# Optimization experiments

Hardware: AMD Instinct MI355X
Metric: run time of the kernel (lower is better)

## Reference

```python
import jax, jax.numpy as jnp
import numpy as np

DIM = 1024
INNER = DIM // 2
DSTATE = 8
KSZ = 3
DTRANK = max(INNER // 8, 4)
B, L = 4, 4096


def setup_inputs() -> dict:
    key = jax.random.key(0)
    ks = jax.random.split(key, 8)
    s = 0.02
    x = jax.random.normal(ks[0], (B, L, DIM), dtype=jnp.float32)
    W_in = jax.random.normal(ks[1], (DIM, DIM), dtype=jnp.float32) * s
    Kx = jax.random.normal(ks[2], (INNER, 1, KSZ), dtype=jnp.float32) * 0.1
    Kz = jax.random.normal(ks[3], (INNER, 1, KSZ), dtype=jnp.float32) * 0.1
    W_xproj = jax.random.normal(ks[4], (DTRANK + 2 * DSTATE, INNER), dtype=jnp.float32) * s
    W_dt = jax.random.normal(ks[5], (INNER, DTRANK), dtype=jnp.float32) * s
    # dt bias: inverse_softplus of exp(linspace(log dt_min, log dt_max))
    dt_init = jnp.exp(jnp.linspace(jnp.log(0.02), jnp.log(0.2), INNER))
    b_dt = jnp.log(jnp.expm1(dt_init)).astype(jnp.float32)
    A_log = jnp.log(jnp.tile(jnp.arange(1, DSTATE + 1, dtype=jnp.float32), (INNER, 1)))
    D = jnp.ones((INNER,), dtype=jnp.float32)
    W_out = jax.random.normal(ks[6], (DIM, DIM), dtype=jnp.float32) * s
    return {"x": x, "W_in": W_in, "Kx": Kx, "Kz": Kz, "W_xproj": W_xproj,
            "W_dt": W_dt, "b_dt": b_dt, "A_log": A_log, "D": D, "W_out": W_out}


def _dwconv_silu(u, kern):
    # u: [B,L,C], kern: [C,1,K] depthwise (groups=C), 'same' padding
    c = u.shape[-1]
    v = jnp.transpose(u, (0, 2, 1))  # [B,C,L]
    v = jax.lax.conv_general_dilated(v, kern, (1,), [(KSZ // 2, KSZ // 2)],
                                     dimension_numbers=("NCH", "OIH", "NCH"),
                                     feature_group_count=c)
    return jax.nn.silu(jnp.transpose(v, (0, 2, 1)))


def _forward(x, W_in, Kx, Kz, W_xproj, W_dt, b_dt, A_log, D, W_out):
    h = jnp.einsum("bld,ed->ble", x, W_in)  # Linear(dim,dim), no bias
    xb, zb = jnp.split(h, 2, axis=-1)       # [B,L,INNER] each
    xb = _dwconv_silu(xb, Kx)
    zb = _dwconv_silu(zb, Kz)
    proj = jnp.einsum("blc,oc->blo", xb, W_xproj)
    dt_raw = proj[..., :DTRANK]
    b_raw = proj[..., DTRANK:DTRANK + DSTATE]
    c_raw = proj[..., DTRANK + DSTATE:]
    delta = jnp.clip(jax.nn.softplus(jnp.einsum("blr,cr->blc", dt_raw, W_dt) + b_dt), 1e-4, 1.0)  # [B,L,C]
    b_term = jnp.tanh(b_raw)  # [B,L,N]
    c_term = jnp.tanh(c_raw)  # [B,L,N]
    a = jax.nn.softplus(A_log) + 1e-4  # [C,N]
    decay = jnp.clip(jnp.exp(-delta[..., None] * a), 1e-4, 1.0)        # [B,L,C,N]
    drive = (1.0 - decay) * (b_term[:, :, None, :] * xb[..., None])    # [B,L,C,N]

    def step(state, inp):
        dec_t, drv_t, c_t, x_t = inp  # [B,C,N], [B,C,N], [B,N], [B,C]
        state = dec_t * state + drv_t
        y = jnp.sum(state * c_t[:, None, :], axis=-1) + D * x_t  # [B,C]
        return state, y

    tm = lambda t: jnp.moveaxis(t, 1, 0)  # time-major
    state0 = jnp.zeros((x.shape[0], INNER, DSTATE), dtype=jnp.float32)
    _, ys = jax.lax.scan(step, state0, (tm(decay), tm(drive), tm(c_term), tm(xb)))
    y = jnp.moveaxis(ys, 0, 1)  # [B,L,INNER]
    return jnp.einsum("bld,ed->ble", jnp.concatenate([y, zb], axis=-1), W_out)


def reference(x, W_in, Kx, Kz, W_xproj, W_dt, b_dt, A_log, D, W_out):
    return _forward(x, W_in, Kx, Kz, W_xproj, W_dt, b_dt, A_log, D, W_out)
```

## Files before the change

### kernel.cpp

```cpp
#include <hip/hip_runtime.h>


using bf16x8 = __attribute__((ext_vector_type(8))) short;
using f32x4  = __attribute__((ext_vector_type(4))) float;

__device__ __forceinline__ unsigned short f2bf(float f) {
  unsigned int u = __float_as_uint(f);
  u = u + 0x7fffu + ((u >> 16) & 1u);
  return (unsigned short)(u >> 16);
}

__device__ __forceinline__ float fsoftplus(float x) {
  return (x > 15.f) ? x : __logf(1.f + __expf(x));
}

__device__ __forceinline__ float ftanh(float x) {
  float v = fminf(fmaxf(x, -15.f), 15.f);
  float e = __expf(2.f * v);
  return (e - 1.f) / (e + 1.f);
}

__global__ __launch_bounds__(256) void cvt_bf16_kernel(
    const float* __restrict__ in, unsigned short* __restrict__ out, int n4) {
  int i = blockIdx.x * 256 + threadIdx.x;
  if (i < n4) {
    float4 v = ((const float4*)in)[i];
    ushort4 o;
    o.x = f2bf(v.x); o.y = f2bf(v.y); o.z = f2bf(v.z); o.w = f2bf(v.w);
    ((ushort4*)out)[i] = o;
  }
}

__global__ __launch_bounds__(256) void cvt_wxp_kernel(
    const float* __restrict__ Wx, unsigned short* __restrict__ out) {
  int i = blockIdx.x * 256 + threadIdx.x;
  int row = i >> 9;
  out[i] = (row < 80) ? f2bf(Wx[i]) : (unsigned short)0;
}

__global__ __launch_bounds__(256) void gemm_bt_bf16(
    const unsigned short* __restrict__ A,
    const unsigned short* __restrict__ B,
    float* __restrict__ C, int M, int N, int K) {
  __shared__ short As[128 * 32];
  __shared__ short Bs[128 * 32];
  const int m0 = blockIdx.x * 128;
  const int n0 = blockIdx.y * 128;
  const int lane = threadIdx.x & 63;
  const int wv = threadIdx.x >> 6;
  const int wm = (wv >> 1) * 64;
  const int wn = (wv & 1) * 64;
  f32x4 acc[4][4] = {};
  const int row_a = wv * 32 + (lane >> 2);
  const int koff = (lane & 3) * 8;
  const unsigned short* gA = A + (size_t)(m0 + row_a) * K + koff;
  const unsigned short* gB = B + (size_t)(n0 + row_a) * K + koff;
  short* lA = &As[(wv * 32) * 32];
  short* lB = &Bs[(wv * 32) * 32];
  const int r = lane & 15;
  const int q = lane >> 4;
  for (int k0 = 0; k0 < K; k0 += 32) {
    __syncthreads();
    __builtin_amdgcn_global_load_lds((const __attribute__((address_space(1))) void*)(const void*)gA,
                                     (__attribute__((address_space(3))) void*)(void*)lA, 16, 0, 0);
    __builtin_amdgcn_global_load_lds((const __attribute__((address_space(1))) void*)(const void*)(gA + 16 * K),
                                     (__attribute__((address_space(3))) void*)(void*)(lA + 16 * 32), 16, 0, 0);
    __builtin_amdgcn_global_load_lds((const __attribute__((address_space(1))) void*)(const void*)gB,
                                     (__attribute__((address_space(3))) void*)(void*)lB, 16, 0, 0);
    __builtin_amdgcn_global_load_lds((const __attribute__((address_space(1))) void*)(const void*)(gB + 16 * K),
                                     (__attribute__((address_space(3))) void*)(void*)(lB + 16 * 32), 16, 0, 0);
    gA += 32; gB += 32;
    __syncthreads();
    bf16x8 av[4], bv[4];
#pragma unroll
    for (int i = 0; i < 4; ++i)
      av[i] = *(const bf16x8*)&As[(wm + i * 16 + r) * 32 + q * 8];
#pragma unroll
    for (int j = 0; j < 4; ++j)
      bv[j] = *(const bf16x8*)&Bs[(wn + j * 16 + r) * 32 + q * 8];
#pragma unroll
    for (int i = 0; i < 4; ++i)
#pragma unroll
      for (int j = 0; j < 4; ++j)
        acc[i][j] = __builtin_amdgcn_mfma_f32_16x16x32_bf16(av[i], bv[j], acc[i][j], 0, 0, 0);
  }
#pragma unroll
  for (int i = 0; i < 4; ++i)
#pragma unroll
    for (int j = 0; j < 4; ++j)
#pragma unroll
      for (int t = 0; t < 4; ++t)
        C[(size_t)(m0 + wm + i * 16 + q * 4 + t) * N + (n0 + wn + j * 16 + r)] = acc[i][j][t];
}

__device__ __forceinline__ void g256_stage(short* lds, int slot,
    const unsigned short* sp, int ktIdx, int wvLds) {
  const unsigned short* s = sp + ktIdx * 64;
  __builtin_amdgcn_global_load_lds((const __attribute__((address_space(1))) void*)s,
      (__attribute__((address_space(3))) void*)(lds + slot * 8192 + wvLds), 16, 0, 0);
  __builtin_amdgcn_global_load_lds((const __attribute__((address_space(1))) void*)(s + 32),
      (__attribute__((address_space(3))) void*)(lds + slot * 8192 + 4096 + wvLds), 16, 0, 0);
}

template <int PAR, int MH, int NHLO, bool RA, bool RB, int SSLOT, bool VM, bool HINT>
__device__ __forceinline__ void g256_phase(
    short* lds, int aSlotOff, int bSlotOff, int aoff, int boff, int wvLds,
    bf16x8 (&av)[4][2], bf16x8 (&bv)[4][2], f32x4 (&acc)[8][4],
    const unsigned short* sp, int ktIdx) {
  if (RA) {
#pragma unroll
    for (int ii = 0; ii < 4; ++ii)
#pragma unroll
      for (int ks = 0; ks < 2; ++ks)
        av[ii][ks] = *(const bf16x8*)&lds[PAR * 4 * 8192 + aSlotOff + ks * 4096 +
                                          (MH * 4 + ii) * 512 + aoff];
  }
  if (RB) {
#pragma unroll
    for (int jj = 0; jj < 2; ++jj)
#pragma unroll
      for (int ks = 0; ks < 2; ++ks)
        bv[NHLO + jj][ks] = *(const bf16x8*)&lds[(PAR * 4 + 2) * 8192 + bSlotOff + ks * 4096 +
                                                 (NHLO + jj) * 512 + boff];
  }
  g256_stage(lds, SSLOT, sp, ktIdx, wvLds);
  if (HINT) asm volatile("s_waitcnt lgkmcnt(8)");
  if (VM) asm volatile("s_waitcnt vmcnt(4)" ::: "memory");
  __builtin_amdgcn_s_barrier();
  asm volatile("s_waitcnt lgkmcnt(0)" ::: "memory");
  __builtin_amdgcn_s_setprio(1);
#pragma unroll
  for (int ii = 0; ii < 4; ++ii)
#pragma unroll
    for (int jj = 0; jj < 2; ++jj) {
      acc[MH * 4 + ii][NHLO + jj] = __builtin_amdgcn_mfma_f32_16x16x32_bf16(
          av[ii][0], bv[NHLO + jj][0], acc[MH * 4 + ii][NHLO + jj], 0, 0, 0);
      acc[MH * 4 + ii][NHLO + jj] = __builtin_amdgcn_mfma_f32_16x16x32_bf16(
          av[ii][1], bv[NHLO + jj][1], acc[MH * 4 + ii][NHLO + jj], 0, 0, 0);
    }
  __builtin_amdgcn_s_setprio(0);
  __builtin_amdgcn_s_barrier();
}

__global__ __launch_bounds__(512, 2) void gemm256_bt(
    const unsigned short* __restrict__ A,
    const unsigned short* __restrict__ B,
    float* __restrict__ C, int M, int N, int K) {
  __shared__ short lds[8 * 8192];
  const int nmt = M >> 8;
  const int bid = blockIdx.x;
  const int swz = (bid & 7) * ((int)gridDim.x >> 3) + (bid >> 3);
  const int mtile = swz % nmt, ntile = swz / nmt;
  const int m0 = mtile << 8, n0 = ntile << 8;
  const int tid = threadIdx.x;
  const int w = tid >> 6, lane = tid & 63;
  const int r = lane & 15, q = lane >> 4;
  const int wrow = w >> 2, wcol = w & 3;
  const int trow = tid >> 2, tcol = (tid & 3) << 3;
  const unsigned short* pA0 = A + (size_t)(m0 + trow) * K + tcol;
  const unsigned short* pA1 = pA0 + (size_t)128 * K;
  const unsigned short* pB0 = B + (size_t)(n0 + trow) * K + tcol;
  const unsigned short* pB1 = pB0 + (size_t)128 * K;
  const int wvLds = w * 512;
  const int aSlotOff = wrow * 8192;
  const int bSlotOff = (wcol >> 1) * 8192;
  const int aoff = r * 32 + q * 8;
  const int boff = (wcol & 1) * 2048 + r * 32 + q * 8;
  bf16x8 av[4][2], bv[4][2];
  f32x4 acc[8][4] = {};
  const int NT = K >> 6;
  const int NI = NT >> 1;
  g256_stage(lds, 0, pA0, 0, wvLds);
  g256_stage(lds, 1, pA1, 0, wvLds);
  g256_stage(lds, 2, pB0, 0, wvLds);
  g256_stage(lds, 3, pB1, 0, wvLds);
  g256_stage(lds, 6, pB0, 1, wvLds);
  g256_stage(lds, 7, pB1, 1, wvLds);
  asm volatile("s_waitcnt vmcnt(4)" ::: "memory");
  __builtin_amdgcn_s_barrier();
#pragma unroll 1
  for (int it = 0; it < NI; ++it) {
    const int ktO  = 2 * it + 1;
    const int ktE2 = (2 * it + 2 < NT) ? 2 * it + 2 : NT - 1;
    const int ktO2 = (2 * it + 3 < NT) ? 2 * it + 3 : NT - 1;
    g256_phase<0, 0, 0, true,  true,  4, false, true >(lds, aSlotOff, bSlotOff, aoff, boff, wvLds, av, bv, acc, pA0, ktO);
    g256_phase<0, 0, 2, false, true,  5, false, false>(lds, aSlotOff, bSlotOff, aoff, boff, wvLds, av, bv, acc, pA1, ktO);
    g256_phase<0, 1, 2, true,  false, 2, false, false>(lds, aSlotOff, bSlotOff, aoff, boff, wvLds, av, bv, acc, pB0, ktE2);
    g256_phase<0, 1, 0, false, false, 0, true,  false>(lds, aSlotOff, bSlotOff, aoff, boff, wvLds, av, bv, acc, pA0, ktE2);
    g256_phase<1, 0, 0, true,  true,  1, false, true >(lds, aSlotOff, bSlotOff, aoff, boff, wvLds, av, bv, acc, pA1, ktE2);
    g256_phase<1, 0, 2, false, true,  3, false, false>(lds, aSlotOff, bSlotOff, aoff, boff, wvLds, av, bv, acc, pB1, ktE2);
    g256_phase<1, 1, 2, true,  false, 6, false, false>(lds, aSlotOff, bSlotOff, aoff, boff, wvLds, av, bv, acc, pB0, ktO2);
    g256_phase<1, 1, 0, false, false, 7, true,  false>(lds, aSlotOff, bSlotOff, aoff, boff, wvLds, av, bv, acc, pB1, ktO2);
  }
  asm volatile("s_waitcnt vmcnt(0) lgkmcnt(0)" ::: "memory");
  float* Cw = C + (size_t)(m0 + wrow * 128) * N + n0 + wcol * 64;
#pragma unroll
  for (int ii = 0; ii < 8; ++ii)
#pragma unroll
    for (int jj = 0; jj < 4; ++jj)
#pragma unroll
      for (int t = 0; t < 4; ++t)
        Cw[(size_t)(ii * 16 + q * 4 + t) * N + jj * 16 + r] = acc[ii][jj][t];
}

__global__ __launch_bounds__(256) void conv_silu_kernel(
    const float* __restrict__ h, const float* __restrict__ Kx, const float* __restrict__ Kz,
    float* __restrict__ xb, unsigned short* __restrict__ xbbf,
    unsigned short* __restrict__ cat) {
  int tid = blockIdx.x * 256 + threadIdx.x;
  int ch = tid & 1023;
  int bl = tid >> 10;
  int l = bl & 4095;
  float k0, k1, k2;
  int c;
  if (ch < 512) { c = ch;       k0 = Kx[c * 3]; k1 = Kx[c * 3 + 1]; k2 = Kx[c * 3 + 2]; }
  else          { c = ch - 512; k0 = Kz[c * 3]; k1 = Kz[c * 3 + 1]; k2 = Kz[c * 3 + 2]; }
  size_t idx = (size_t)bl * 1024 + ch;
  float um = (l > 0)    ? h[idx - 1024] : 0.f;
  float u0 = h[idx];
  float up = (l < 4095) ? h[idx + 1024] : 0.f;
  float v = um * k0 + u0 * k1 + up * k2;
  float o = v / (1.f + __expf(-v));
  if (ch < 512) { xb[(size_t)bl * 512 + c] = o; xbbf[(size_t)bl * 512 + c] = f2bf(o); }
  else          cat[idx] = f2bf(o);
}

__global__ __launch_bounds__(256) void prep_dtbc_kernel(
    const float* __restrict__ proj, unsigned short* __restrict__ dtr,
    float* __restrict__ bterm, float* __restrict__ cterm) {
  int i = blockIdx.x * 256 + threadIdx.x;
  int row = i >> 7, col = i & 127;
  float v = proj[i];
  if (col < 64)      dtr[row * 64 + col] = f2bf(v);
  else if (col < 72) bterm[row * 8 + (col - 64)] = ftanh(v);
  else if (col < 80) cterm[row * 8 + (col - 72)] = ftanh(v);
}

__global__ __launch_bounds__(256) void scan_p1(
    const float* __restrict__ draw, const float* __restrict__ bterm,
    const float* __restrict__ xb, const float* __restrict__ A_log,
    const float* __restrict__ bdt,
    float* __restrict__ Aprod, float* __restrict__ Bpart) {
  int tid = threadIdx.x;
  int gid = blockIdx.x;
  int chunk = gid & 127, half = (gid >> 7) & 1, b = gid >> 8;
  int c = half * 256 + tid;
  float4 a0 = *(const float4*)&A_log[c * 8];
  float4 a1 = *(const float4*)&A_log[c * 8 + 4];
  float na[8] = {a0.x, a0.y, a0.z, a0.w, a1.x, a1.y, a1.z, a1.w};
#pragma unroll
  for (int s = 0; s < 8; ++s) na[s] = -(fsoftplus(na[s]) + 1e-4f);
  float bb = bdt[c];
  int l0 = chunk * 32;
  size_t base  = ((size_t)b * 4096 + l0) * 512 + c;
  size_t bbase = ((size_t)b * 4096 + l0) * 8;
  float S[8] = {}, Ap[8] = {1.f, 1.f, 1.f, 1.f, 1.f, 1.f, 1.f, 1.f};
  for (int i = 0; i < 32; ++i) {
    float dr = draw[base] + bb;
    float xv = xb[base];
    float delta = fminf(fmaxf(fsoftplus(dr), 1e-4f), 1.f);
    float4 bt0 = *(const float4*)&bterm[bbase];
    float4 bt1 = *(const float4*)&bterm[bbase + 4];
    float bt[8] = {bt0.x, bt0.y, bt0.z, bt0.w, bt1.x, bt1.y, bt1.z, bt1.w};
#pragma unroll
    for (int s = 0; s < 8; ++s) {
      float dec = fminf(fmaxf(__expf(delta * na[s]), 1e-4f), 1.f);
      float btx = bt[s] * xv;
      S[s] = dec * S[s] + (btx - dec * btx);
      Ap[s] *= dec;
    }
    base += 512; bbase += 8;
  }
  size_t o = (size_t)chunk * 16384 + ((size_t)(b * 512 + c)) * 8;
  *(float4*)&Aprod[o]     = make_float4(Ap[0], Ap[1], Ap[2], Ap[3]);
  *(float4*)&Aprod[o + 4] = make_float4(Ap[4], Ap[5], Ap[6], Ap[7]);
  *(float4*)&Bpart[o]     = make_float4(S[0], S[1], S[2], S[3]);
  *(float4*)&Bpart[o + 4] = make_float4(S[4], S[5], S[6], S[7]);
}

__global__ __launch_bounds__(256) void scan_p2(
    const float* __restrict__ Aprod, const float* __restrict__ Bpart,
    float* __restrict__ initst) {
  int t = blockIdx.x * 256 + threadIdx.x;
  float st = 0.f;
  for (int ch = 0; ch < 128; ++ch) {
    size_t o = (size_t)ch * 16384 + t;
    initst[o] = st;
    st = Aprod[o] * st + Bpart[o];
  }
}

__global__ __launch_bounds__(256) void scan_p3(
    const float* __restrict__ draw, const float* __restrict__ bterm,
    const float* __restrict__ cterm, const float* __restrict__ xb,
    const float* __restrict__ A_log, const float* __restrict__ bdt,
    const float* __restrict__ Dp,
    const float* __restrict__ initst, unsigned short* __restrict__ cat) {
  int tid = threadIdx.x;
  int gid = blockIdx.x;
  int chunk = gid & 127, half = (gid >> 7) & 1, b = gid >> 8;
  int c = half * 256 + tid;
  float4 a0 = *(const float4*)&A_log[c * 8];
  float4 a1 = *(const float4*)&A_log[c * 8 + 4];
  float na[8] = {a0.x, a0.y, a0.z, a0.w, a1.x, a1.y, a1.z, a1.w};
#pragma unroll
  for (int s = 0; s < 8; ++s) na[s] = -(fsoftplus(na[s]) + 1e-4f);
  float bb = bdt[c];
  float Dv = Dp[c];
  size_t o = (size_t)chunk * 16384 + ((size_t)(b * 512 + c)) * 8;
  float4 s0 = *(const float4*)&initst[o];
  float4 s1 = *(const float4*)&initst[o + 4];
  float S[8] = {s0.x, s0.y, s0.z, s0.w, s1.x, s1.y, s1.z, s1.w};
  int l0 = chunk * 32;
  size_t base  = ((size_t)b * 4096 + l0) * 512 + c;
  size_t bbase = ((size_t)b * 4096 + l0) * 8;
  size_t cbase = ((size_t)b * 4096 + l0) * 1024 + c;
  for (int i = 0; i < 32; ++i) {
    float dr = draw[base] + bb;
    float xv = xb[base];
    float delta = fminf(fmaxf(fsoftplus(dr), 1e-4f), 1.f);
    float4 bt0 = *(const float4*)&bterm[bbase];
    float4 bt1 = *(const float4*)&bterm[bbase + 4];
    float4 ct0 = *(const float4*)&cterm[bbase];
    float4 ct1 = *(const float4*)&cterm[bbase + 4];
    float bt[8] = {bt0.x, bt0.y, bt0.z, bt0.w, bt1.x, bt1.y, bt1.z, bt1.w};
    float ct[8] = {ct0.x, ct0.y, ct0.z, ct0.w, ct1.x, ct1.y, ct1.z, ct1.w};
    float acc = Dv * xv;
#pragma unroll
    for (int s = 0; s < 8; ++s) {
      float dec = fminf(fmaxf(__expf(delta * na[s]), 1e-4f), 1.f);
      float btx = bt[s] * xv;
      S[s] = dec * S[s] + (btx - dec * btx);
      acc += S[s] * ct[s];
    }
    cat[cbase] = f2bf(acc);
    base += 512; bbase += 8; cbase += 1024;
  }
}

extern "C" void kernel_launch(void* const* d_in, const int* in_sizes, int n_in,
                              void* d_out, int out_size, void* d_ws, size_t ws_size,
                              hipStream_t stream) {
  (void)in_sizes; (void)n_in; (void)out_size; (void)ws_size;
  const float* x       = (const float*)d_in[0];
  const float* W_in    = (const float*)d_in[1];
  const float* Kx      = (const float*)d_in[2];
  const float* Kz      = (const float*)d_in[3];
  const float* W_xproj = (const float*)d_in[4];
  const float* W_dt    = (const float*)d_in[5];
  const float* b_dt    = (const float*)d_in[6];
  const float* A_log   = (const float*)d_in[7];
  const float* Dp      = (const float*)d_in[8];
  const float* W_out   = (const float*)d_in[9];
  float* out = (float*)d_out;

  char* w = (char*)d_ws;
  unsigned short* xbf  = (unsigned short*)(w);
  float* xb    = (float*)(w + 33554432);
  float* draw  = (float*)(w + 67108864);
  float* bterm = (float*)(w + 100663296);
  float* cterm = (float*)(w + 101187584);
  float* Aprod = (float*)(w + 101711872);
  float* Bpart = (float*)(w + 110100480);
  float* initst = (float*)(w + 118489088);
  unsigned short* winbf  = (unsigned short*)(w + 126877696);
  unsigned short* woutbf = (unsigned short*)(w + 128974848);
  unsigned short* dtr    = (unsigned short*)(w + 131072000);
  unsigned short* wxp_bf = (unsigned short*)(w + 133169152);
  unsigned short* wd_bf  = (unsigned short*)(w + 133300224);
  unsigned short* xbbf = (unsigned short*)Aprod;
  float* proj = draw;
  float* h = out;

  cvt_bf16_kernel<<<16384, 256, 0, stream>>>(x, xbf, 4194304);
  cvt_bf16_kernel<<<1024, 256, 0, stream>>>(W_in, winbf, 262144);
  cvt_bf16_kernel<<<1024, 256, 0, stream>>>(W_out, woutbf, 262144);
  cvt_bf16_kernel<<<32, 256, 0, stream>>>(W_dt, wd_bf, 8192);
  cvt_wxp_kernel<<<256, 256, 0, stream>>>(W_xproj, wxp_bf);

  gemm256_bt<<<256, 512, 0, stream>>>(xbf, winbf, h, 16384, 1024, 1024);

  conv_silu_kernel<<<65536, 256, 0, stream>>>(h, Kx, Kz, xb, xbbf, xbf );

  gemm_bt_bf16<<<dim3(128, 1), 256, 0, stream>>>(xbbf, wxp_bf, proj, 16384, 128, 512);
  prep_dtbc_kernel<<<8192, 256, 0, stream>>>(proj, dtr, bterm, cterm);
  gemm_bt_bf16<<<dim3(128, 4), 256, 0, stream>>>(dtr, wd_bf, draw, 16384, 512, 64);

  scan_p1<<<1024, 256, 0, stream>>>(draw, bterm, xb, A_log, b_dt, Aprod, Bpart);
  scan_p2<<<64, 256, 0, stream>>>(Aprod, Bpart, initst);
  scan_p3<<<1024, 256, 0, stream>>>(draw, bterm, cterm, xb, A_log, b_dt, Dp, initst, xbf );

  gemm256_bt<<<256, 512, 0, stream>>>(xbf, woutbf, out, 16384, 1024, 1024);
}
```

Measured before the change: 351.6 us.

## Swizzle LDS layout for 256-tile GEMM staging and remap tiles per XCD

The GEMM staging now loads full 64-wide K rows per thread group and XOR-swizzles the column chunk by row. The fragment reads apply the matching swizzle, which is meant to cut LDS bank conflicts on the bf16x8 reads and make the global loads more contiguous. Block-to-tile mapping changes so each XCD owns a contiguous band of M tiles, aiming for better L2 reuse. This assumes nmt is divisible by 8, and the new layout has to stay exactly consistent between the stage and read paths.

```diff
diff --git a/kernel.cpp b/kernel.cpp
--- a/kernel.cpp
+++ b/kernel.cpp
@@ -94,11 +94,11 @@
 }
 
 __device__ __forceinline__ void g256_stage(short* lds, int slot,
-    const unsigned short* sp, int ktIdx, int wvLds) {
+    const unsigned short* sp, int ktIdx, int wvLds, int K) {
   const unsigned short* s = sp + ktIdx * 64;
   __builtin_amdgcn_global_load_lds((const __attribute__((address_space(1))) void*)s,
       (__attribute__((address_space(3))) void*)(lds + slot * 8192 + wvLds), 16, 0, 0);
-  __builtin_amdgcn_global_load_lds((const __attribute__((address_space(1))) void*)(s + 32),
+  __builtin_amdgcn_global_load_lds((const __attribute__((address_space(1))) void*)(s + (size_t)64 * K),
       (__attribute__((address_space(3))) void*)(lds + slot * 8192 + 4096 + wvLds), 16, 0, 0);
 }
 
@@ -106,24 +106,22 @@
 __device__ __forceinline__ void g256_phase(
     short* lds, int aSlotOff, int bSlotOff, int aoff, int boff, int wvLds,
     bf16x8 (&av)[4][2], bf16x8 (&bv)[4][2], f32x4 (&acc)[8][4],
-    const unsigned short* sp, int ktIdx) {
+    const unsigned short* sp, int ktIdx, int K) {
   if (RA) {
 #pragma unroll
-    for (int ii = 0; ii < 4; ++ii)
-#pragma unroll
-      for (int ks = 0; ks < 2; ++ks)
-        av[ii][ks] = *(const bf16x8*)&lds[PAR * 4 * 8192 + aSlotOff + ks * 4096 +
-                                          (MH * 4 + ii) * 512 + aoff];
+    for (int ii = 0; ii < 4; ++ii) {
+      av[ii][0] = *(const bf16x8*)&lds[PAR * 4 * 8192 + aSlotOff + MH * 4096 + ii * 1024 + aoff];
+      av[ii][1] = *(const bf16x8*)&lds[PAR * 4 * 8192 + aSlotOff + MH * 4096 + ii * 1024 + (aoff ^ 32)];
+    }
   }
   if (RB) {
 #pragma unroll
-    for (int jj = 0; jj < 2; ++jj)
-#pragma unroll
-      for (int ks = 0; ks < 2; ++ks)
-        bv[NHLO + jj][ks] = *(const bf16x8*)&lds[(PAR * 4 + 2) * 8192 + bSlotOff + ks * 4096 +
-                                                 (NHLO + jj) * 512 + boff];
-  }
-  g256_stage(lds, SSLOT, sp, ktIdx, wvLds);
+    for (int jj = 0; jj < 2; ++jj) {
+      bv[NHLO + jj][0] = *(const bf16x8*)&lds[(PAR * 4 + 2) * 8192 + bSlotOff + (NHLO + jj) * 1024 + boff];
+      bv[NHLO + jj][1] = *(const bf16x8*)&lds[(PAR * 4 + 2) * 8192 + bSlotOff + (NHLO + jj) * 1024 + (boff ^ 32)];
+    }
+  }
+  g256_stage(lds, SSLOT, sp, ktIdx, wvLds, K);
   if (HINT) asm volatile("s_waitcnt lgkmcnt(8)");
   if (VM) asm volatile("s_waitcnt vmcnt(4)" ::: "memory");
   __builtin_amdgcn_s_barrier();
@@ -149,33 +147,38 @@
   __shared__ short lds[8 * 8192];
   const int nmt = M >> 8;
   const int bid = blockIdx.x;
-  const int swz = (bid & 7) * ((int)gridDim.x >> 3) + (bid >> 3);
-  const int mtile = swz % nmt, ntile = swz / nmt;
+  const int g = nmt >> 3;
+  const int xcd = bid & 7;
+  const int loc = bid >> 3;
+  const int mtile = xcd * g + (loc % g);
+  const int ntile = loc / g;
   const int m0 = mtile << 8, n0 = ntile << 8;
   const int tid = threadIdx.x;
   const int w = tid >> 6, lane = tid & 63;
   const int r = lane & 15, q = lane >> 4;
   const int wrow = w >> 2, wcol = w & 3;
-  const int trow = tid >> 2, tcol = (tid & 3) << 3;
-  const unsigned short* pA0 = A + (size_t)(m0 + trow) * K + tcol;
-  const unsigned short* pA1 = pA0 + (size_t)128 * K;
-  const unsigned short* pB0 = B + (size_t)(n0 + trow) * K + tcol;
-  const unsigned short* pB1 = pB0 + (size_t)128 * K;
+  const int srow = tid >> 3;
+  const int scol = ((tid & 7) ^ (srow & 7)) << 3;
+  const unsigned short* pA0 = A + (size_t)(m0 + srow) * K + scol;
+  const unsigned short* pA1 = A + (size_t)(m0 + 128 + srow) * K + scol;
+  const unsigned short* pB0 = B + (size_t)(n0 + srow) * K + scol;
+  const unsigned short* pB1 = B + (size_t)(n0 + 128 + srow) * K + scol;
   const int wvLds = w * 512;
   const int aSlotOff = wrow * 8192;
   const int bSlotOff = (wcol >> 1) * 8192;
-  const int aoff = r * 32 + q * 8;
-  const int boff = (wcol & 1) * 2048 + r * 32 + q * 8;
+  const int swzc = (q * 8) ^ ((r & 7) << 3);
+  const int aoff = r * 64 + swzc;
+  const int boff = (wcol & 1) * 4096 + r * 64 + swzc;
   bf16x8 av[4][2], bv[4][2];
   f32x4 acc[8][4] = {};
   const int NT = K >> 6;
   const int NI = NT >> 1;
-  g256_stage(lds, 0, pA0, 0, wvLds);
-  g256_stage(lds, 1, pA1, 0, wvLds);
-  g256_stage(lds, 2, pB0, 0, wvLds);
-  g256_stage(lds, 3, pB1, 0, wvLds);
-  g256_stage(lds, 6, pB0, 1, wvLds);
-  g256_stage(lds, 7, pB1, 1, wvLds);
+  g256_stage(lds, 0, pA0, 0, wvLds, K);
+  g256_stage(lds, 1, pA1, 0, wvLds, K);
+  g256_stage(lds, 2, pB0, 0, wvLds, K);
+  g256_stage(lds, 3, pB1, 0, wvLds, K);
+  g256_stage(lds, 6, pB0, 1, wvLds, K);
+  g256_stage(lds, 7, pB1, 1, wvLds, K);
   asm volatile("s_waitcnt vmcnt(4)" ::: "memory");
   __builtin_amdgcn_s_barrier();
 #pragma unroll 1
@@ -183,14 +186,14 @@
     const int ktO  = 2 * it + 1;
     const int ktE2 = (2 * it + 2 < NT) ? 2 * it + 2 : NT - 1;
     const int ktO2 = (2 * it + 3 < NT) ? 2 * it + 3 : NT - 1;
-    g256_phase<0, 0, 0, true,  true,  4, false, true >(lds, aSlotOff, bSlotOff, aoff, boff, wvLds, av, bv, acc, pA0, ktO);
-    g256_phase<0, 0, 2, false, true,  5, false, false>(lds, aSlotOff, bSlotOff, aoff, boff, wvLds, av, bv, acc, pA1, ktO);
-    g256_phase<0, 1, 2, true,  false, 2, false, false>(lds, aSlotOff, bSlotOff, aoff, boff, wvLds, av, bv, acc, pB0, ktE2);
-    g256_phase<0, 1, 0, false, false, 0, true,  false>(lds, aSlotOff, bSlotOff, aoff, boff, wvLds, av, bv, acc, pA0, ktE2);
-    g256_phase<1, 0, 0, true,  true,  1, false, true >(lds, aSlotOff, bSlotOff, aoff, boff, wvLds, av, bv, acc, pA1, ktE2);
-    g256_phase<1, 0, 2, false, true,  3, false, false>(lds, aSlotOff, bSlotOff, aoff, boff, wvLds, av, bv, acc, pB1, ktE2);
-    g256_phase<1, 1, 2, true,  false, 6, false, false>(lds, aSlotOff, bSlotOff, aoff, boff, wvLds, av, bv, acc, pB0, ktO2);
-    g256_phase<1, 1, 0, false, false, 7, true,  false>(lds, aSlotOff, bSlotOff, aoff, boff, wvLds, av, bv, acc, pB1, ktO2);
+    g256_phase<0, 0, 0, true,  true,  4, false, true >(lds, aSlotOff, bSlotOff, aoff, boff, wvLds, av, bv, acc, pA0, ktO,  K);
+    g256_phase<0, 0, 2, false, true,  5, false, false>(lds, aSlotOff, bSlotOff, aoff, boff, wvLds, av, bv, acc, pA1, ktO,  K);
+    g256_phase<0, 1, 2, true,  false, 2, false, false>(lds, aSlotOff, bSlotOff, aoff, boff, wvLds, av, bv, acc, pB0, ktE2, K);
+    g256_phase<0, 1, 0, false, false, 0, true,  false>(lds, aSlotOff, bSlotOff, aoff, boff, wvLds, av, bv, acc, pA0, ktE2, K);
+    g256_phase<1, 0, 0, true,  true,  1, false, true >(lds, aSlotOff, bSlotOff, aoff, boff, wvLds, av, bv, acc, pA1, ktE2, K);
+    g256_phase<1, 0, 2, false, true,  3, false, false>(lds, aSlotOff, bSlotOff, aoff, boff, wvLds, av, bv, acc, pB1, ktE2, K);
+    g256_phase<1, 1, 2, true,  false, 6, false, false>(lds, aSlotOff, bSlotOff, aoff, boff, wvLds, av, bv, acc, pB0, ktO2, K);
+    g256_phase<1, 1, 0, false, false, 7, true,  false>(lds, aSlotOff, bSlotOff, aoff, boff, wvLds, av, bv, acc, pB1, ktO2, K);
   }
   asm volatile("s_waitcnt vmcnt(0) lgkmcnt(0)" ::: "memory");
   float* Cw = C + (size_t)(m0 + wrow * 128) * N + n0 + wcol * 64;
```

Result: no change. 347.5 us (-1.2%).
